# Optimization experiments

Hardware: AMD Instinct MI355X
Metric: run time of the kernel (lower is better)

Reference implementation:

```python
import jax, jax.numpy as jnp
import numpy as np

N_HEADS = 8
N_LANDMARKS = 64
NEWTON_ITERS = 6


def _iterative_inv(mat):
    # mat: [B,H,L,L]; Newton-Schulz approximate inverse, 6 iterations
    L = mat.shape[-1]
    fro = jnp.sqrt(jnp.sum(mat * mat, axis=(-2, -1), keepdims=True))
    fro = jnp.maximum(fro, 1e-6)
    z = jnp.swapaxes(mat, -2, -1) / (fro * fro)
    for _ in range(NEWTON_ITERS):
        z = 2.0 * z - z @ mat @ z
    return z


def setup_inputs() -> dict:
    key = jax.random.key(0)
    ks = jax.random.split(key, 5)
    B, N, C = 4, 8192, 512
    s = 1.0 / np.sqrt(C)
    return {
        "x": jax.random.normal(ks[0], (B, N, C), jnp.float32),
        "Wqkv": jax.random.normal(ks[1], (3 * C, C), jnp.float32) * s,
        "bqkv": jax.random.normal(ks[2], (3 * C,), jnp.float32) * 0.01,
        "Wproj": jax.random.normal(ks[3], (C, C), jnp.float32) * s,
        "bproj": jax.random.normal(ks[4], (C,), jnp.float32) * 0.01,
    }


def reference(x, Wqkv, bqkv, Wproj, bproj):
    B, N, C = x.shape
    H = N_HEADS
    hd = C // H
    scale = hd ** (-0.5)
    n_lm = N_LANDMARKS

    qkv = x @ Wqkv.T + bqkv                       # [B,N,3C]
    qkv = qkv.reshape(B, N, 3, H, hd).transpose(2, 0, 3, 1, 4)  # [3,B,H,N,hd]
    q, k, v = qkv[0], qkv[1], qkv[2]

    if N <= n_lm:
        attn = jax.nn.softmax(q @ jnp.swapaxes(k, -2, -1) * scale, axis=-1)
        out = attn @ v
    else:
        stride = max(N // n_lm, 1)
        lm_idx = jnp.arange(0, N, stride)[:n_lm]
        q_lm = q[:, :, lm_idx]                    # [B,H,L,hd]
        k_lm = k[:, :, lm_idx]
        kernel_1 = jax.nn.softmax(q @ jnp.swapaxes(k_lm, -2, -1) * scale, axis=-1)   # [B,H,N,L]
        kernel_2 = jax.nn.softmax(q_lm @ jnp.swapaxes(k_lm, -2, -1) * scale, axis=-1)  # [B,H,L,L]
        kernel_3 = jax.nn.softmax(q_lm @ jnp.swapaxes(k, -2, -1) * scale, axis=-1)   # [B,H,L,N]
        kernel_2_inv = _iterative_inv(kernel_2)
        out = kernel_1 @ (kernel_2_inv @ (kernel_3 @ v))  # [B,H,N,hd]

    out = jnp.swapaxes(out, 1, 2).reshape(B, N, C)
    return out @ Wproj.T + bproj
```

## Files before the change

### kernel.cpp

```cpp
#include <hip/hip_runtime.h>

typedef unsigned short u16;
typedef unsigned int u32;

typedef __bf16 v8bf __attribute__((ext_vector_type(8)));
typedef float v4f __attribute__((ext_vector_type(4)));
typedef u16 v8u __attribute__((ext_vector_type(8)));

#define N_TOK 8192
#define CDIM 512
#define HEADS 8
#define HD 64
#define LM 64
#define LSTRIDE 128
#define BHN 32
#define NCHUNK 16
#define SCALE 0.125f

__device__ __forceinline__ float b2f(u16 u) { return __uint_as_float(((u32)u) << 16); }
__device__ __forceinline__ u16 f2bf(float f) {
  u32 u = __float_as_uint(f);
  u += 0x7fffu + ((u >> 16) & 1u);
  return (u16)(u >> 16);
}
__device__ __forceinline__ u32 pk2bf(float a, float b) {
  return (u32)f2bf(a) | ((u32)f2bf(b) << 16);
}

__device__ __forceinline__ void gl_lds16(const u16* g, u16* l) {
  __builtin_amdgcn_global_load_lds(
      (const __attribute__((address_space(1))) u32*)g,
      (__attribute__((address_space(3))) u32*)l, 16, 0, 0);
}

__global__ __launch_bounds__(256) void cast_bf16(const float* __restrict__ src,
                                                 u16* __restrict__ dst, int n8) {
  int i = blockIdx.x * 256 + threadIdx.x;
  if (i >= n8) return;
  const float4* s = (const float4*)src;
  float4 a = s[(size_t)i * 2], b = s[(size_t)i * 2 + 1];
  uint4 o;
  o.x = (u32)f2bf(a.x) | ((u32)f2bf(a.y) << 16);
  o.y = (u32)f2bf(a.z) | ((u32)f2bf(a.w) << 16);
  o.z = (u32)f2bf(b.x) | ((u32)f2bf(b.y) << 16);
  o.w = (u32)f2bf(b.z) | ((u32)f2bf(b.w) << 16);
  *(uint4*)(dst + (size_t)i * 8) = o;
}

template <int MODE>
__global__ __launch_bounds__(512) void gemm_bt(const u16* __restrict__ A,
                                               const u16* __restrict__ Bm,
                                               const float* __restrict__ bias,
                                               u16* __restrict__ qo,
                                               u16* __restrict__ ko,
                                               u16* __restrict__ vo,
                                               float* __restrict__ outp) {
  __shared__ __align__(16) u16 Al[16384];
  __shared__ __align__(16) u16 Bl[16384];
  const int K = 512;
  const int NT = 16;
  const int m0 = blockIdx.x * 256;
  const int n0 = blockIdx.y * 256;
  const int t = threadIdx.x;
  const int lane = t & 63, w = t >> 6;
  const int wm = w >> 2, wn = w & 3;
  const int quad = lane >> 4, lrow = lane & 15;
  const int rslot = (quad ^ ((lrow >> 1) & 3)) * 8;

  const int srl = t >> 2, slt = t & 3;
  const int gch = (slt ^ ((srl >> 1) & 3)) * 8;
  const int rA0 = ((srl >> 6) & 1) * 128 + (srl & 63);
  const int rB0 = ((srl >> 5) & 3) * 64 + (srl & 31);

#define STAGE_A(tt, qg, bb)                                                  \
  gl_lds16(A + (size_t)(m0 + rA0 + (qg) * 64) * K + (tt) * 32 + gch,         \
           &Al[(bb) * 8192 + (qg) * 4096 + t * 8])
#define STAGE_B(tt, qg, bb)                                                  \
  gl_lds16(Bm + (size_t)(n0 + rB0 + (qg) * 32) * K + (tt) * 32 + gch,        \
           &Bl[(bb) * 8192 + (qg) * 4096 + t * 8])

  v4f acc[8][4];
#pragma unroll
  for (int i = 0; i < 8; ++i)
#pragma unroll
    for (int j = 0; j < 4; ++j)
#pragma unroll
      for (int r = 0; r < 4; ++r) acc[i][j][r] = 0.f;

  STAGE_A(0, 0, 0); STAGE_B(0, 0, 0);
  STAGE_A(0, 1, 0); STAGE_B(0, 1, 0);
  STAGE_A(1, 0, 1); STAGE_B(1, 0, 1);

  v8bf af[4], b0[2], b1[2];
#pragma unroll 2
  for (int u = 0; u < NT; ++u) {
    const int bu = u & 1, bn = bu ^ 1;
    const u16* Ab = &Al[bu * 8192];
    const u16* Bb = &Bl[bu * 8192];
    asm volatile("s_waitcnt vmcnt(2)" ::: "memory");
    __builtin_amdgcn_s_barrier();
    __builtin_amdgcn_sched_barrier(0);
#pragma unroll
    for (int ml = 0; ml < 4; ++ml)
      af[ml] = *(const v8bf*)&Ab[(wm * 64 + ml * 16 + lrow) * 32 + rslot];
#pragma unroll
    for (int nl = 0; nl < 2; ++nl)
      b0[nl] = *(const v8bf*)&Bb[(wn * 32 + nl * 16 + lrow) * 32 + rslot];
    if (u + 1 < NT) STAGE_A(u + 1, 1, bn);
    __builtin_amdgcn_sched_barrier(0);
    __builtin_amdgcn_s_barrier();
    __builtin_amdgcn_sched_barrier(0);
    __builtin_amdgcn_s_setprio(1);
#pragma unroll
    for (int ml = 0; ml < 4; ++ml)
#pragma unroll
      for (int nl = 0; nl < 2; ++nl)
        acc[ml][nl] = __builtin_amdgcn_mfma_f32_16x16x32_bf16(af[ml], b0[nl], acc[ml][nl], 0, 0, 0);
    __builtin_amdgcn_s_setprio(0);
    __builtin_amdgcn_s_barrier();
#pragma unroll
    for (int nl = 0; nl < 2; ++nl)
      b1[nl] = *(const v8bf*)&Bb[4096 + (wn * 32 + nl * 16 + lrow) * 32 + rslot];
    if (u + 1 < NT) STAGE_B(u + 1, 1, bn);
    __builtin_amdgcn_sched_barrier(0);
    __builtin_amdgcn_s_barrier();
    __builtin_amdgcn_sched_barrier(0);
    __builtin_amdgcn_s_setprio(1);
#pragma unroll
    for (int ml = 0; ml < 4; ++ml)
#pragma unroll
      for (int nl = 0; nl < 2; ++nl)
        acc[ml][2 + nl] = __builtin_amdgcn_mfma_f32_16x16x32_bf16(af[ml], b1[nl], acc[ml][2 + nl], 0, 0, 0);
    __builtin_amdgcn_s_setprio(0);
    __builtin_amdgcn_s_barrier();
#pragma unroll
    for (int ml = 0; ml < 4; ++ml)
      af[ml] = *(const v8bf*)&Ab[4096 + (wm * 64 + ml * 16 + lrow) * 32 + rslot];
    if (u + 2 < NT) STAGE_A(u + 2, 0, bu);
    __builtin_amdgcn_sched_barrier(0);
    __builtin_amdgcn_s_barrier();
    __builtin_amdgcn_sched_barrier(0);
    __builtin_amdgcn_s_setprio(1);
#pragma unroll
    for (int ml = 0; ml < 4; ++ml)
#pragma unroll
      for (int nl = 0; nl < 2; ++nl)
        acc[4 + ml][nl] = __builtin_amdgcn_mfma_f32_16x16x32_bf16(af[ml], b0[nl], acc[4 + ml][nl], 0, 0, 0);
    __builtin_amdgcn_s_setprio(0);
    __builtin_amdgcn_s_barrier();
    if (u + 2 < NT) STAGE_B(u + 2, 0, bu);
    __builtin_amdgcn_sched_barrier(0);
    __builtin_amdgcn_s_barrier();
    __builtin_amdgcn_sched_barrier(0);
    __builtin_amdgcn_s_setprio(1);
#pragma unroll
    for (int ml = 0; ml < 4; ++ml)
#pragma unroll
      for (int nl = 0; nl < 2; ++nl)
        acc[4 + ml][2 + nl] = __builtin_amdgcn_mfma_f32_16x16x32_bf16(af[ml], b1[nl], acc[4 + ml][2 + nl], 0, 0, 0);
    __builtin_amdgcn_s_setprio(0);
    __builtin_amdgcn_s_barrier();
  }
#undef STAGE_A
#undef STAGE_B

#pragma unroll
  for (int mf = 0; mf < 8; ++mf) {
#pragma unroll
    for (int nf = 0; nf < 4; ++nf) {
      int gn = n0 + wn * 64 + nf * 16 + lrow;
      float bv = bias[gn];
#pragma unroll
      for (int r = 0; r < 4; ++r) {
        int gm = m0 + wm * 128 + mf * 16 + quad * 4 + r;
        float val = acc[mf][nf][r] + bv;
        if (MODE == 0) {
          int tt = gn >> 9;
          int h = (gn >> 6) & 7;
          int d = gn & 63;
          int b = gm >> 13;
          int n = gm & 8191;
          size_t di = ((size_t)(b * HEADS + h) * N_TOK + n) * HD + d;
          u16* dst = (tt == 0) ? qo : (tt == 1) ? ko : vo;
          dst[di] = f2bf(val);
        } else {
          outp[(size_t)gm * CDIM + gn] = val;
        }
      }
    }
  }
}

__global__ __launch_bounds__(256) void fpart(const u16* __restrict__ qb,
                                             const u16* __restrict__ kb,
                                             const u16* __restrict__ vb,
                                             float* __restrict__ Fp,
                                             float* __restrict__ Mc,
                                             float* __restrict__ Sc) {
  __shared__ __align__(16) char smem[4 * 64 * 40 * 2 * 2];
  __shared__ float msh[4][64], ssh[4][64];
  const int jc = blockIdx.x, bh = blockIdx.y;
  const int t = threadIdx.x;
  const int lane = t & 63, w = t >> 6;
  const int col = lane & 15, quad = lane >> 4;
  const int jq = lane & 7, dh = lane >> 3;

  u16* Pw = (u16*)smem + w * (64 * 40);
  u16* vT = (u16*)smem + 4 * (64 * 40) + w * (64 * 40);
  float* Fbuf = (float*)smem;

  v8bf qf[4][2];
#pragma unroll
  for (int it = 0; it < 4; ++it)
#pragma unroll
    for (int kh = 0; kh < 2; ++kh)
      qf[it][kh] = *(const v8bf*)(qb + ((size_t)bh * N_TOK + (size_t)(it * 16 + col) * LSTRIDE) * HD + kh * 32 + quad * 8);

  float mw[4], sw[4];
  v4f facc[4][4];
#pragma unroll
  for (int it = 0; it < 4; ++it) { mw[it] = -3.0e38f; sw[it] = 0.f; }
#pragma unroll
  for (int dt = 0; dt < 4; ++dt)
#pragma unroll
    for (int it = 0; it < 4; ++it)
#pragma unroll
      for (int r = 0; r < 4; ++r) facc[dt][it][r] = 0.f;

  for (int st = 0; st < 4; ++st) {
    const int j0 = jc * 512 + w * 128 + st * 32;

    v8bf kf[2][2];
#pragma unroll
    for (int jt = 0; jt < 2; ++jt)
#pragma unroll
      for (int kh = 0; kh < 2; ++kh)
        kf[jt][kh] = *(const v8bf*)(kb + ((size_t)bh * N_TOK + j0 + jt * 16 + col) * HD + kh * 32 + quad * 8);

    v8u r0 = *(const v8u*)(vb + ((size_t)bh * N_TOK + j0 + jq * 4 + 0) * HD + dh * 8);
    v8u r1 = *(const v8u*)(vb + ((size_t)bh * N_TOK + j0 + jq * 4 + 1) * HD + dh * 8);
    v8u r2 = *(const v8u*)(vb + ((size_t)bh * N_TOK + j0 + jq * 4 + 2) * HD + dh * 8);
    v8u r3 = *(const v8u*)(vb + ((size_t)bh * N_TOK + j0 + jq * 4 + 3) * HD + dh * 8);
#pragma unroll
    for (int e = 0; e < 8; ++e) {
      uint2 pk;
      pk.x = (u32)r0[e] | ((u32)r1[e] << 16);
      pk.y = (u32)r2[e] | ((u32)r3[e] << 16);
      *(uint2*)&vT[(dh * 8 + e) * 40 + jq * 4] = pk;
    }

    v4f sacc[2][4];
#pragma unroll
    for (int jt = 0; jt < 2; ++jt)
#pragma unroll
      for (int it = 0; it < 4; ++it) {
#pragma unroll
        for (int r = 0; r < 4; ++r) sacc[jt][it][r] = 0.f;
#pragma unroll
        for (int kh = 0; kh < 2; ++kh)
          sacc[jt][it] = __builtin_amdgcn_mfma_f32_16x16x32_bf16(kf[jt][kh], qf[it][kh], sacc[jt][it], 0, 0, 0);
      }

#pragma unroll
    for (int it = 0; it < 4; ++it) {
      float mloc = -3.0e38f;
#pragma unroll
      for (int jt = 0; jt < 2; ++jt)
#pragma unroll
        for (int r = 0; r < 4; ++r) {
          float s = sacc[jt][it][r] * SCALE;
          sacc[jt][it][r] = s;
          mloc = fmaxf(mloc, s);
        }
      mloc = fmaxf(mloc, __shfl_xor(mloc, 16));
      mloc = fmaxf(mloc, __shfl_xor(mloc, 32));
      float mnew = fmaxf(mw[it], mloc);
      float alpha = __expf(mw[it] - mnew);
      mw[it] = mnew;
      float rs = 0.f;
#pragma unroll
      for (int jt = 0; jt < 2; ++jt)
#pragma unroll
        for (int r = 0; r < 4; ++r) {
          float p = __expf(sacc[jt][it][r] - mnew);
          sacc[jt][it][r] = p;
          rs += p;
        }
      rs += __shfl_xor(rs, 16);
      rs += __shfl_xor(rs, 32);
      sw[it] = sw[it] * alpha + rs;
#pragma unroll
      for (int jt = 0; jt < 2; ++jt) {
        uint2 pk;
        pk.x = pk2bf(sacc[jt][it][0], sacc[jt][it][1]);
        pk.y = pk2bf(sacc[jt][it][2], sacc[jt][it][3]);
        *(uint2*)&Pw[(it * 16 + col) * 40 + jt * 16 + quad * 4] = pk;
      }
#pragma unroll
      for (int dt = 0; dt < 4; ++dt)
#pragma unroll
        for (int r = 0; r < 4; ++r) facc[dt][it][r] *= alpha;
    }

    v8bf vfr[4], pfr[4];
#pragma unroll
    for (int dt = 0; dt < 4; ++dt)
      vfr[dt] = *(const v8bf*)&vT[(dt * 16 + col) * 40 + quad * 8];
#pragma unroll
    for (int it = 0; it < 4; ++it)
      pfr[it] = *(const v8bf*)&Pw[(it * 16 + col) * 40 + quad * 8];
#pragma unroll
    for (int dt = 0; dt < 4; ++dt)
#pragma unroll
      for (int it = 0; it < 4; ++it)
        facc[dt][it] = __builtin_amdgcn_mfma_f32_16x16x32_bf16(vfr[dt], pfr[it], facc[dt][it], 0, 0, 0);
  }

  if (quad == 0) {
#pragma unroll
    for (int it = 0; it < 4; ++it) {
      msh[w][it * 16 + col] = mw[it];
      ssh[w][it * 16 + col] = sw[it];
    }
  }
  __syncthreads();

  const size_t cb = (size_t)(bh * NCHUNK + jc) * 64;
  float scl[4];
#pragma unroll
  for (int it = 0; it < 4; ++it) {
    int i = it * 16 + col;
    float m0 = msh[0][i], m1 = msh[1][i], m2 = msh[2][i], m3 = msh[3][i];
    float M = fmaxf(fmaxf(m0, m1), fmaxf(m2, m3));
    float e0 = __expf(m0 - M), e1 = __expf(m1 - M);
    float e2 = __expf(m2 - M), e3 = __expf(m3 - M);
    float Stot = e0 * ssh[0][i] + e1 * ssh[1][i] + e2 * ssh[2][i] + e3 * ssh[3][i];
    scl[it] = (w == 0) ? e0 : (w == 1) ? e1 : (w == 2) ? e2 : e3;
    if (w == 0 && quad == 0) {
      Mc[cb + i] = M;
      Sc[cb + i] = Stot;
    }
  }

  for (int wv = 0; wv < 4; ++wv) {
    if (w == wv) {
#pragma unroll
      for (int it = 0; it < 4; ++it)
#pragma unroll
        for (int dt = 0; dt < 4; ++dt) {
          float* dst = &Fbuf[(it * 16 + col) * 76 + dt * 16 + quad * 4];
          float4 v;
          v.x = facc[dt][it][0] * scl[it];
          v.y = facc[dt][it][1] * scl[it];
          v.z = facc[dt][it][2] * scl[it];
          v.w = facc[dt][it][3] * scl[it];
          if (wv == 0) {
            *(float4*)dst = v;
          } else {
            float4 o = *(float4*)dst;
            o.x += v.x; o.y += v.y; o.z += v.z; o.w += v.w;
            *(float4*)dst = o;
          }
        }
    }
    __syncthreads();
  }

  size_t base = (size_t)(bh * NCHUNK + jc) * 4096;
#pragma unroll
  for (int p = 0; p < 16; ++p) {
    int idx = p * 256 + t;
    Fp[base + idx] = Fbuf[(idx >> 6) * 76 + (idx & 63)];
  }
}

__global__ __launch_bounds__(256) void newton_t(const u16* __restrict__ qb,
                                                const u16* __restrict__ kb,
                                                const float* __restrict__ Fp,
                                                const float* __restrict__ Mc,
                                                const float* __restrict__ Sc,
                                                u16* __restrict__ Tt) {
  __shared__ float Ms[4096];
  __shared__ float Z0s[4096];
  __shared__ float Ws[4096];
  __shared__ float Xs[4096];
  const int bh = blockIdx.x;
  const int t = threadIdx.x;
  const int lane = t & 63, w = t >> 6;
  const int ti = t >> 4, tj = t & 15;

#pragma unroll
  for (int p = 0; p < 16; ++p) {
    int idx = p * 256 + t;
    int i = idx >> 6, d = idx & 63;
    Ws[idx] = b2f(qb[((size_t)bh * N_TOK + i * LSTRIDE) * HD + d]);
    Xs[d * 64 + i] = b2f(kb[((size_t)bh * N_TOK + i * LSTRIDE) * HD + d]);
  }
  __syncthreads();

  {
    float a2[4][4];
#pragma unroll
    for (int a = 0; a < 4; ++a)
#pragma unroll
      for (int b = 0; b < 4; ++b) a2[a][b] = 0.f;
    for (int d = 0; d < 64; ++d) {
      float qa[4], kv[4];
#pragma unroll
      for (int a = 0; a < 4; ++a) qa[a] = Ws[(ti * 4 + a) * 64 + d];
#pragma unroll
      for (int b = 0; b < 4; ++b) kv[b] = Xs[d * 64 + tj * 4 + b];
#pragma unroll
      for (int a = 0; a < 4; ++a)
#pragma unroll
        for (int b = 0; b < 4; ++b) a2[a][b] += qa[a] * kv[b];
    }
    __syncthreads();
#pragma unroll
    for (int a = 0; a < 4; ++a)
#pragma unroll
      for (int b = 0; b < 4; ++b) Ms[(ti * 4 + a) * 64 + tj * 4 + b] = a2[a][b] * SCALE;
  }
  __syncthreads();

  for (int rr = 0; rr < 16; ++rr) {
    int i = w * 16 + rr;
    float vv = Ms[i * 64 + lane];
    float m = vv;
#pragma unroll
    for (int off = 32; off; off >>= 1) m = fmaxf(m, __shfl_xor(m, off));
    float e = expf(vv - m);
    float s = e;
#pragma unroll
    for (int off = 32; off; off >>= 1) s += __shfl_xor(s, off);
    Ms[i * 64 + lane] = e / s;
  }
  __syncthreads();

  float loc = 0.f;
#pragma unroll
  for (int p = 0; p < 16; ++p) {
    float v = Ms[p * 256 + t];
    loc += v * v;
  }
#pragma unroll
  for (int off = 32; off; off >>= 1) loc += __shfl_xor(loc, off);
  if (lane == 0) Z0s[w] = loc;
  __syncthreads();
  float fro = fmaxf(sqrtf(Z0s[0] + Z0s[1] + Z0s[2] + Z0s[3]), 1e-6f);
  float invden = 1.0f / (fro * fro);
  __syncthreads();

#pragma unroll
  for (int p = 0; p < 16; ++p) {
    int idx = p * 256 + t;
    int i = idx >> 6, j = idx & 63;
    Z0s[j * 64 + i] = Ms[idx] * invden;
  }
  __syncthreads();

  float* Z = Z0s;
  float* Zn = Xs;
  for (int it = 0; it < 6; ++it) {
    {
      float a2[4][4];
#pragma unroll
      for (int a = 0; a < 4; ++a)
#pragma unroll
        for (int b = 0; b < 4; ++b) a2[a][b] = 0.f;
      for (int tt = 0; tt < 64; ++tt) {
        float za[4], mb[4];
#pragma unroll
        for (int a = 0; a < 4; ++a) za[a] = Z[(ti * 4 + a) * 64 + tt];
#pragma unroll
        for (int b = 0; b < 4; ++b) mb[b] = Ms[tt * 64 + tj * 4 + b];
#pragma unroll
        for (int a = 0; a < 4; ++a)
#pragma unroll
          for (int b = 0; b < 4; ++b) a2[a][b] += za[a] * mb[b];
      }
#pragma unroll
      for (int a = 0; a < 4; ++a)
#pragma unroll
        for (int b = 0; b < 4; ++b) Ws[(ti * 4 + a) * 64 + tj * 4 + b] = a2[a][b];
    }
    __syncthreads();
    {
      float a2[4][4];
#pragma unroll
      for (int a = 0; a < 4; ++a)
#pragma unroll
        for (int b = 0; b < 4; ++b) a2[a][b] = 0.f;
      for (int tt = 0; tt < 64; ++tt) {
        float wa[4], zb[4];
#pragma unroll
        for (int a = 0; a < 4; ++a) wa[a] = Ws[(ti * 4 + a) * 64 + tt];
#pragma unroll
        for (int b = 0; b < 4; ++b) zb[b] = Z[tt * 64 + tj * 4 + b];
#pragma unroll
        for (int a = 0; a < 4; ++a)
#pragma unroll
          for (int b = 0; b < 4; ++b) a2[a][b] += wa[a] * zb[b];
      }
#pragma unroll
      for (int a = 0; a < 4; ++a)
#pragma unroll
        for (int b = 0; b < 4; ++b)
          Zn[(ti * 4 + a) * 64 + tj * 4 + b] =
              2.f * Z[(ti * 4 + a) * 64 + tj * 4 + b] - a2[a][b];
    }
    __syncthreads();
    float* tmp = Z; Z = Zn; Zn = tmp;
  }

  float* wts = Ms;
  if (t < 64) {
    float M = -3.0e38f;
#pragma unroll
    for (int jc = 0; jc < NCHUNK; ++jc)
      M = fmaxf(M, Mc[(bh * NCHUNK + jc) * 64 + t]);
    float S = 0.f;
#pragma unroll
    for (int jc = 0; jc < NCHUNK; ++jc)
      S += expf(Mc[(bh * NCHUNK + jc) * 64 + t] - M) * Sc[(bh * NCHUNK + jc) * 64 + t];
    float invS = 1.0f / S;
#pragma unroll
    for (int jc = 0; jc < NCHUNK; ++jc)
      wts[jc * 64 + t] = expf(Mc[(bh * NCHUNK + jc) * 64 + t] - M) * invS;
  }
  __syncthreads();

#pragma unroll
  for (int p = 0; p < 16; ++p) {
    int idx = p * 256 + t;
    int i = idx >> 6;
    float sum = 0.f;
#pragma unroll
    for (int jc = 0; jc < NCHUNK; ++jc)
      sum += wts[jc * 64 + i] * Fp[(size_t)(bh * NCHUNK + jc) * 4096 + idx];
    Ws[idx] = sum;
  }
  __syncthreads();

  {
    float a2[4][4];
#pragma unroll
    for (int a = 0; a < 4; ++a)
#pragma unroll
      for (int b = 0; b < 4; ++b) a2[a][b] = 0.f;
    for (int tt = 0; tt < 64; ++tt) {
      float za[4], fb[4];
#pragma unroll
      for (int a = 0; a < 4; ++a) za[a] = Z[(ti * 4 + a) * 64 + tt];
#pragma unroll
      for (int b = 0; b < 4; ++b) fb[b] = Ws[tt * 64 + tj * 4 + b];
#pragma unroll
      for (int a = 0; a < 4; ++a)
#pragma unroll
        for (int b = 0; b < 4; ++b) a2[a][b] += za[a] * fb[b];
    }
#pragma unroll
    for (int a = 0; a < 4; ++a)
#pragma unroll
      for (int b = 0; b < 4; ++b)
        Tt[(size_t)bh * 4096 + (size_t)(tj * 4 + b) * 64 + (ti * 4 + a)] = f2bf(a2[a][b]);
  }
}

__global__ __launch_bounds__(256) void attn_out_k(const u16* __restrict__ qb,
                                                  const u16* __restrict__ kb,
                                                  const u16* __restrict__ Tt,
                                                  u16* __restrict__ ao) {
  __shared__ __align__(16) u16 Pl[4][1024];
  const int bh = blockIdx.y;
  const int b = bh >> 3, h = bh & 7;
  const int t = threadIdx.x;
  const int lane = t & 63, w = t >> 6;
  const int col = lane & 15, quad = lane >> 4;
  const int rot = (col & 7) * 8;

  v8bf kfr[4][2], tfr[4][2];
#pragma unroll
  for (int tj = 0; tj < 4; ++tj)
#pragma unroll
    for (int kh = 0; kh < 2; ++kh)
      kfr[tj][kh] = *(const v8bf*)(kb + ((size_t)bh * N_TOK + (size_t)(tj * 16 + col) * LSTRIDE) * HD + kh * 32 + quad * 8);
#pragma unroll
  for (int td = 0; td < 4; ++td)
#pragma unroll
    for (int jh = 0; jh < 2; ++jh)
      tfr[td][jh] = *(const v8bf*)(Tt + (size_t)bh * 4096 + (size_t)(td * 16 + col) * 64 + jh * 32 + quad * 8);

  u16* Pw = &Pl[w][0];

  for (int tile = 0; tile < 4; ++tile) {
    const int n0 = blockIdx.x * 256 + w * 64 + tile * 16;
    v8bf qf[2];
#pragma unroll
    for (int kh = 0; kh < 2; ++kh)
      qf[kh] = *(const v8bf*)(qb + ((size_t)bh * N_TOK + n0 + col) * HD + kh * 32 + quad * 8);

    v4f S[4];
#pragma unroll
    for (int tj = 0; tj < 4; ++tj) {
#pragma unroll
      for (int r = 0; r < 4; ++r) S[tj][r] = 0.f;
#pragma unroll
      for (int kh = 0; kh < 2; ++kh)
        S[tj] = __builtin_amdgcn_mfma_f32_16x16x32_bf16(kfr[tj][kh], qf[kh], S[tj], 0, 0, 0);
    }

    float mx = -3.0e38f;
#pragma unroll
    for (int tj = 0; tj < 4; ++tj)
#pragma unroll
      for (int r = 0; r < 4; ++r) {
        S[tj][r] *= SCALE;
        mx = fmaxf(mx, S[tj][r]);
      }
    mx = fmaxf(mx, __shfl_xor(mx, 16));
    mx = fmaxf(mx, __shfl_xor(mx, 32));
    float sum = 0.f;
#pragma unroll
    for (int tj = 0; tj < 4; ++tj)
#pragma unroll
      for (int r = 0; r < 4; ++r) {
        S[tj][r] = __expf(S[tj][r] - mx);
        sum += S[tj][r];
      }
    sum += __shfl_xor(sum, 16);
    sum += __shfl_xor(sum, 32);
    float inv = 1.0f / sum;

#pragma unroll
    for (int tj = 0; tj < 4; ++tj) {
      u32 lo = (u32)f2bf(S[tj][0] * inv) | ((u32)f2bf(S[tj][1] * inv) << 16);
      u32 hi = (u32)f2bf(S[tj][2] * inv) | ((u32)f2bf(S[tj][3] * inv) << 16);
      uint2 pk = {lo, hi};
      *(uint2*)&Pw[col * 64 + ((tj * 16 + quad * 4 + rot) & 63)] = pk;
    }
    v8bf pf[2];
#pragma unroll
    for (int jh = 0; jh < 2; ++jh)
      pf[jh] = *(const v8bf*)&Pw[col * 64 + ((jh * 32 + quad * 8 + rot) & 63)];

    v4f O[4];
#pragma unroll
    for (int td = 0; td < 4; ++td) {
#pragma unroll
      for (int r = 0; r < 4; ++r) O[td][r] = 0.f;
#pragma unroll
      for (int jh = 0; jh < 2; ++jh)
        O[td] = __builtin_amdgcn_mfma_f32_16x16x32_bf16(pf[jh], tfr[td][jh], O[td], 0, 0, 0);
    }
#pragma unroll
    for (int td = 0; td < 4; ++td)
#pragma unroll
      for (int r = 0; r < 4; ++r) {
        int n = n0 + quad * 4 + r;
        ao[((size_t)(b * N_TOK + n)) * CDIM + h * HD + td * 16 + col] = f2bf(O[td][r]);
      }
  }
}

__global__ void ws_too_small_sentinel(float* out) {
  if (threadIdx.x == 0 && blockIdx.x == 0) out[0] = 1.0f;
}

static constexpr size_t SZ_QKV = (size_t)BHN * N_TOK * HD * 2;
static constexpr size_t OFF_Q = 0;
static constexpr size_t OFF_K = OFF_Q + SZ_QKV;
static constexpr size_t OFF_V = OFF_K + SZ_QKV;
static constexpr size_t OFF_FP = OFF_V + SZ_QKV;
static constexpr size_t SZ_FP = (size_t)BHN * NCHUNK * 4096 * 4;
static constexpr size_t OFF_MC = OFF_FP + SZ_FP;
static constexpr size_t SZ_MS = (size_t)BHN * NCHUNK * 64 * 4;
static constexpr size_t OFF_SC = OFF_MC + SZ_MS;
static constexpr size_t OFF_T = OFF_SC + SZ_MS;
static constexpr size_t OFF_WQ = OFF_T + (size_t)BHN * 4096 * 2;
static constexpr size_t OFF_WP = OFF_WQ + (size_t)3 * CDIM * CDIM * 2;
static constexpr size_t OFF_END = OFF_WP + (size_t)CDIM * CDIM * 2;

extern "C" void kernel_launch(void* const* d_in, const int* in_sizes, int n_in,
                              void* d_out, int out_size, void* d_ws, size_t ws_size,
                              hipStream_t stream) {
  const float* x = (const float*)d_in[0];
  const float* Wqkv = (const float*)d_in[1];
  const float* bqkv = (const float*)d_in[2];
  const float* Wproj = (const float*)d_in[3];
  const float* bproj = (const float*)d_in[4];
  float* out = (float*)d_out;
  char* ws = (char*)d_ws;
  if (ws_size < OFF_END) {
    ws_too_small_sentinel<<<1, 64, 0, stream>>>(out);
    return;
  }

  u16* qb = (u16*)(ws + OFF_Q);
  u16* kb = (u16*)(ws + OFF_K);
  u16* vb = (u16*)(ws + OFF_V);
  float* Fp = (float*)(ws + OFF_FP);
  float* Mc = (float*)(ws + OFF_MC);
  float* Sc = (float*)(ws + OFF_SC);
  u16* Tt = (u16*)(ws + OFF_T);
  u16* Wqb = (u16*)(ws + OFF_WQ);
  u16* Wpb = (u16*)(ws + OFF_WP);
  u16* attn = (u16*)(ws + OFF_V);
  u16* xb = (u16*)d_out;

  cast_bf16<<<8192, 256, 0, stream>>>(x, xb, 2097152);
  cast_bf16<<<384, 256, 0, stream>>>(Wqkv, Wqb, 98304);
  cast_bf16<<<128, 256, 0, stream>>>(Wproj, Wpb, 32768);
  gemm_bt<0><<<dim3(128, 6), 512, 0, stream>>>(xb, Wqb, bqkv, qb, kb, vb, nullptr);
  fpart<<<dim3(NCHUNK, BHN), 256, 0, stream>>>(qb, kb, vb, Fp, Mc, Sc);
  newton_t<<<dim3(BHN), 256, 0, stream>>>(qb, kb, Fp, Mc, Sc, Tt);
  attn_out_k<<<dim3(32, BHN), 256, 0, stream>>>(qb, kb, Tt, attn);
  gemm_bt<1><<<dim3(128, 2), 512, 0, stream>>>(attn, Wpb, bproj, nullptr, nullptr, nullptr, out);
}
```

Measured before the change: 313.1 us.

## Double GEMM K-tile to 64 with reworked 8-phase LDS staging and swizzle

The QKV/projection GEMM now stages K-tiles of 64 instead of 32, halving the number of main-loop iterations and barrier groups. LDS buffers double to 128KB total, the XOR swizzle changes to an 8-chunk pattern, and the prefetch schedule is reordered across four sub-phases with explicit lgkmcnt waits. Launch bounds request 2 blocks per CU, but the larger LDS footprint likely limits occupancy, and the extra waits may reduce overlap.

```diff
diff --git a/kernel.cpp b/kernel.cpp
--- a/kernel.cpp
+++ b/kernel.cpp
@@ -48,36 +48,34 @@
 }
 
 template <int MODE>
-__global__ __launch_bounds__(512) void gemm_bt(const u16* __restrict__ A,
-                                               const u16* __restrict__ Bm,
-                                               const float* __restrict__ bias,
-                                               u16* __restrict__ qo,
-                                               u16* __restrict__ ko,
-                                               u16* __restrict__ vo,
-                                               float* __restrict__ outp) {
-  __shared__ __align__(16) u16 Al[16384];
-  __shared__ __align__(16) u16 Bl[16384];
+__global__ __launch_bounds__(512, 2) void gemm_bt(const u16* __restrict__ A,
+                                                  const u16* __restrict__ Bm,
+                                                  const float* __restrict__ bias,
+                                                  u16* __restrict__ qo,
+                                                  u16* __restrict__ ko,
+                                                  u16* __restrict__ vo,
+                                                  float* __restrict__ outp) {
+  __shared__ __align__(16) u16 Al[32768];
+  __shared__ __align__(16) u16 Bl[32768];
   const int K = 512;
-  const int NT = 16;
+  const int NT = 8;
   const int m0 = blockIdx.x * 256;
   const int n0 = blockIdx.y * 256;
   const int t = threadIdx.x;
   const int lane = t & 63, w = t >> 6;
   const int wm = w >> 2, wn = w & 3;
   const int quad = lane >> 4, lrow = lane & 15;
-  const int rslot = (quad ^ ((lrow >> 1) & 3)) * 8;
-
-  const int srl = t >> 2, slt = t & 3;
-  const int gch = (slt ^ ((srl >> 1) & 3)) * 8;
-  const int rA0 = ((srl >> 6) & 1) * 128 + (srl & 63);
-  const int rB0 = ((srl >> 5) & 3) * 64 + (srl & 31);
-
-#define STAGE_A(tt, qg, bb)                                                  \
-  gl_lds16(A + (size_t)(m0 + rA0 + (qg) * 64) * K + (tt) * 32 + gch,         \
-           &Al[(bb) * 8192 + (qg) * 4096 + t * 8])
-#define STAGE_B(tt, qg, bb)                                                  \
-  gl_lds16(Bm + (size_t)(n0 + rB0 + (qg) * 32) * K + (tt) * 32 + gch,        \
-           &Bl[(bb) * 8192 + (qg) * 4096 + t * 8])
+  const int l3 = lrow & 7;
+
+  const int srl = t >> 3;
+  const int gch = ((t & 7) ^ (srl & 7)) * 8;
+
+#define STA(g, tt)                                                            \
+  gl_lds16(A + (size_t)(m0 + (g) * 64 + srl) * K + (tt) * 64 + gch,           \
+           &Al[((tt) & 1) * 16384 + (g) * 4096 + t * 8])
+#define STB(g, tt)                                                            \
+  gl_lds16(Bm + (size_t)(n0 + (g) * 64 + srl) * K + (tt) * 64 + gch,          \
+           &Bl[((tt) & 1) * 16384 + (g) * 4096 + t * 8])
 
   v4f acc[8][4];
 #pragma unroll
@@ -87,82 +85,105 @@
 #pragma unroll
       for (int r = 0; r < 4; ++r) acc[i][j][r] = 0.f;
 
-  STAGE_A(0, 0, 0); STAGE_B(0, 0, 0);
-  STAGE_A(0, 1, 0); STAGE_B(0, 1, 0);
-  STAGE_A(1, 0, 1); STAGE_B(1, 0, 1);
-
-  v8bf af[4], b0[2], b1[2];
-#pragma unroll 2
-  for (int u = 0; u < NT; ++u) {
-    const int bu = u & 1, bn = bu ^ 1;
-    const u16* Ab = &Al[bu * 8192];
-    const u16* Bb = &Bl[bu * 8192];
-    asm volatile("s_waitcnt vmcnt(2)" ::: "memory");
+  STA(0, 0); STA(2, 0); STB(0, 0); STB(1, 0); STA(1, 0); STA(3, 0);
+  STB(2, 0); STB(3, 0);
+  STA(0, 1); STA(2, 1); STB(0, 1); STB(1, 1); STA(1, 1); STA(3, 1);
+
+  v8bf af[4][2], b0[2][2], b1[2][2];
+  for (int S = 0; S < NT; ++S) {
+    const int bu = S & 1;
+    const u16* Ab = &Al[bu * 16384];
+    const u16* Bb = &Bl[bu * 16384];
+    asm volatile("s_waitcnt vmcnt(6)" ::: "memory");
     __builtin_amdgcn_s_barrier();
     __builtin_amdgcn_sched_barrier(0);
 #pragma unroll
-    for (int ml = 0; ml < 4; ++ml)
-      af[ml] = *(const v8bf*)&Ab[(wm * 64 + ml * 16 + lrow) * 32 + rslot];
-#pragma unroll
-    for (int nl = 0; nl < 2; ++nl)
-      b0[nl] = *(const v8bf*)&Bb[(wn * 32 + nl * 16 + lrow) * 32 + rslot];
-    if (u + 1 < NT) STAGE_A(u + 1, 1, bn);
+    for (int fm = 0; fm < 4; ++fm)
+#pragma unroll
+      for (int kk = 0; kk < 2; ++kk)
+        af[fm][kk] = *(const v8bf*)&Ab[(wm * 128 + fm * 16 + lrow) * 64 +
+                                       (((kk * 4 + quad) ^ l3) * 8)];
+#pragma unroll
+    for (int fn = 0; fn < 2; ++fn)
+#pragma unroll
+      for (int kk = 0; kk < 2; ++kk)
+        b0[fn][kk] = *(const v8bf*)&Bb[(wn * 64 + fn * 16 + lrow) * 64 +
+                                       (((kk * 4 + quad) ^ l3) * 8)];
+    if (S + 1 < NT) { STB(2, S + 1); STB(3, S + 1); }
     __builtin_amdgcn_sched_barrier(0);
     __builtin_amdgcn_s_barrier();
+    asm volatile("s_waitcnt lgkmcnt(0)" ::: "memory");
     __builtin_amdgcn_sched_barrier(0);
     __builtin_amdgcn_s_setprio(1);
 #pragma unroll
-    for (int ml = 0; ml < 4; ++ml)
-#pragma unroll
-      for (int nl = 0; nl < 2; ++nl)
-        acc[ml][nl] = __builtin_amdgcn_mfma_f32_16x16x32_bf16(af[ml], b0[nl], acc[ml][nl], 0, 0, 0);
+    for (int fm = 0; fm < 4; ++fm)
+#pragma unroll
+      for (int fn = 0; fn < 2; ++fn)
+#pragma unroll
+        for (int kk = 0; kk < 2; ++kk)
+          acc[fm][fn] = __builtin_amdgcn_mfma_f32_16x16x32_bf16(af[fm][kk], b0[fn][kk], acc[fm][fn], 0, 0, 0);
     __builtin_amdgcn_s_setprio(0);
+    __builtin_amdgcn_sched_barrier(0);
     __builtin_amdgcn_s_barrier();
 #pragma unroll
-    for (int nl = 0; nl < 2; ++nl)
-      b1[nl] = *(const v8bf*)&Bb[4096 + (wn * 32 + nl * 16 + lrow) * 32 + rslot];
-    if (u + 1 < NT) STAGE_B(u + 1, 1, bn);
+    for (int fn = 0; fn < 2; ++fn)
+#pragma unroll
+      for (int kk = 0; kk < 2; ++kk)
+        b1[fn][kk] = *(const v8bf*)&Bb[(wn * 64 + 32 + fn * 16 + lrow) * 64 +
+                                       (((kk * 4 + quad) ^ l3) * 8)];
+    if (S + 2 < NT) { STA(0, S + 2); STA(2, S + 2); }
     __builtin_amdgcn_sched_barrier(0);
     __builtin_amdgcn_s_barrier();
+    asm volatile("s_waitcnt lgkmcnt(0)" ::: "memory");
     __builtin_amdgcn_sched_barrier(0);
     __builtin_amdgcn_s_setprio(1);
 #pragma unroll
-    for (int ml = 0; ml < 4; ++ml)
-#pragma unroll
-      for (int nl = 0; nl < 2; ++nl)
-        acc[ml][2 + nl] = __builtin_amdgcn_mfma_f32_16x16x32_bf16(af[ml], b1[nl], acc[ml][2 + nl], 0, 0, 0);
+    for (int fm = 0; fm < 4; ++fm)
+#pragma unroll
+      for (int fn = 0; fn < 2; ++fn)
+#pragma unroll
+        for (int kk = 0; kk < 2; ++kk)
+          acc[fm][2 + fn] = __builtin_amdgcn_mfma_f32_16x16x32_bf16(af[fm][kk], b1[fn][kk], acc[fm][2 + fn], 0, 0, 0);
     __builtin_amdgcn_s_setprio(0);
+    __builtin_amdgcn_sched_barrier(0);
     __builtin_amdgcn_s_barrier();
 #pragma unroll
-    for (int ml = 0; ml < 4; ++ml)
-      af[ml] = *(const v8bf*)&Ab[4096 + (wm * 64 + ml * 16 + lrow) * 32 + rslot];
-    if (u + 2 < NT) STAGE_A(u + 2, 0, bu);
+    for (int fm = 0; fm < 4; ++fm)
+#pragma unroll
+      for (int kk = 0; kk < 2; ++kk)
+        af[fm][kk] = *(const v8bf*)&Ab[(wm * 128 + 64 + fm * 16 + lrow) * 64 +
+                                       (((kk * 4 + quad) ^ l3) * 8)];
+    if (S + 2 < NT) { STB(0, S + 2); STB(1, S + 2); }
     __builtin_amdgcn_sched_barrier(0);
     __builtin_amdgcn_s_barrier();
+    asm volatile("s_waitcnt lgkmcnt(0)" ::: "memory");
     __builtin_amdgcn_sched_barrier(0);
     __builtin_amdgcn_s_setprio(1);
 #pragma unroll
-    for (int ml = 0; ml < 4; ++ml)
-#pragma unroll
-      for (int nl = 0; nl < 2; ++nl)
-        acc[4 + ml][nl] = __builtin_amdgcn_mfma_f32_16x16x32_bf16(af[ml], b0[nl], acc[4 + ml][nl], 0, 0, 0);
+    for (int fm = 0; fm < 4; ++fm)
+#pragma unroll
+      for (int fn = 0; fn < 2; ++fn)
+#pragma unroll
+        for (int kk = 0; kk < 2; ++kk)
+          acc[4 + fm][fn] = __builtin_amdgcn_mfma_f32_16x16x32_bf16(af[fm][kk], b0[fn][kk], acc[4 + fm][fn], 0, 0, 0);
     __builtin_amdgcn_s_setprio(0);
+    __builtin_amdgcn_sched_barrier(0);
     __builtin_amdgcn_s_barrier();
-    if (u + 2 < NT) STAGE_B(u + 2, 0, bu);
-    __builtin_amdgcn_sched_barrier(0);
-    __builtin_amdgcn_s_barrier();
+    if (S + 2 < NT) { STA(1, S + 2); STA(3, S + 2); }
     __builtin_amdgcn_sched_barrier(0);
     __builtin_amdgcn_s_setprio(1);
 #pragma unroll
-    for (int ml = 0; ml < 4; ++ml)
-#pragma unroll
-      for (int nl = 0; nl < 2; ++nl)
-        acc[4 + ml][2 + nl] = __builtin_amdgcn_mfma_f32_16x16x32_bf16(af[ml], b1[nl], acc[4 + ml][2 + nl], 0, 0, 0);
+    for (int fm = 0; fm < 4; ++fm)
+#pragma unroll
+      for (int fn = 0; fn < 2; ++fn)
+#pragma unroll
+        for (int kk = 0; kk < 2; ++kk)
+          acc[4 + fm][2 + fn] = __builtin_amdgcn_mfma_f32_16x16x32_bf16(af[fm][kk], b1[fn][kk], acc[4 + fm][2 + fn], 0, 0, 0);
     __builtin_amdgcn_s_setprio(0);
-    __builtin_amdgcn_s_barrier();
-  }
-#undef STAGE_A
-#undef STAGE_B
+    __builtin_amdgcn_sched_barrier(0);
+  }
+#undef STA
+#undef STB
 
 #pragma unroll
   for (int mf = 0; mf < 8; ++mf) {
```

Measured after the change: 358.0 us. 14.4% more time.
